# Performance work log

Hardware: AMD Instinct MI355X
Metric: run time of the kernel (lower is better)

The kernel has to match this reference:

```python
import jax, jax.numpy as jnp
import numpy as np

# ---- constants (from init_kwargs / Config) ----
C = 10            # number of classes
P = 128           # fixed prototype capacity per class (masked)
GAMMA = 0.1
B_CONST = 10.0    # b
TAO = 1.0
BETA = 1.0
LAMBDA = 0.1
THRESHOLD = 40.0
EPS = 1e-6        # nn.PairwiseDistance eps (added to the difference)


def setup_inputs() -> dict:
    key = jax.random.key(0)
    k1, k2 = jax.random.split(key)
    features = jax.random.normal(k1, (8192, 512), dtype=jnp.float32)
    labels = jax.random.randint(k2, (8192,), 0, C, dtype=jnp.int32)
    return {"features": features, "labels": labels}


def _assign_prototypes(features, labels):
    """Sequential prototype assignment (faithful to assign_prototype).
    Fixed-capacity store: protos [C,P,D], counts [C,P], nproto [C]."""
    D = features.shape[1]
    protos = jnp.zeros((C, P, D), features.dtype)
    counts = jnp.zeros((C, P), jnp.int32)
    nproto = jnp.zeros((C,), jnp.int32)

    def step(carry, xs):
        protos, counts, nproto = carry
        f, l = xs
        row = protos[l]                       # [P, D]
        cnt = counts[l]                       # [P]
        n = nproto[l]
        valid = jnp.arange(P) < n
        d2 = jnp.sum((f[None, :] - row + EPS) ** 2, axis=-1)
        d2m = jnp.where(valid, d2, jnp.inf)
        idx = jnp.argmin(d2m)
        dmin = jnp.sqrt(d2m[idx])
        do_update = (n > 0) & (dmin < THRESHOLD)
        # running-mean update of closest prototype
        c = cnt[idx].astype(f.dtype)
        new_val = (row[idx] * c + f) / (c + 1.0)
        app_idx = jnp.minimum(n, P - 1)       # append slot (clamped; never hit with these settings)
        tgt_idx = jnp.where(do_update, idx, app_idx)
        tgt_val = jnp.where(do_update, new_val, f)
        tgt_cnt = jnp.where(do_update, cnt[idx] + 1, 1)
        row = row.at[tgt_idx].set(tgt_val)
        cnt = cnt.at[tgt_idx].set(tgt_cnt)
        n = jnp.where(do_update, n, jnp.minimum(n + 1, P))
        protos = protos.at[l].set(row)
        counts = counts.at[l].set(cnt)
        nproto = nproto.at[l].set(n)
        return (protos, counts, nproto), None

    (protos, counts, nproto), _ = jax.lax.scan(step, (protos, counts, nproto), (features, labels))
    return protos, nproto


def _forward(features, labels):
    # assign_prototype uses tensor(features).detach() -> stop_gradient
    protos, nproto = _assign_prototypes(jax.lax.stop_gradient(features), labels)
    B, D = features.shape
    flat = protos.reshape(C * P, D)
    valid = (jnp.arange(P)[None, :] < nproto[:, None]).reshape(C * P)

    # squared PairwiseDistance with eps added to the difference:
    # sum((f - p + eps)^2) = |f|^2 + |p|^2 - 2 f.p + 2*eps*(sum f - sum p) + D*eps^2
    f2 = jnp.sum(features ** 2, axis=-1)          # [B]
    p2 = jnp.sum(flat ** 2, axis=-1)              # [C*P]
    sf = jnp.sum(features, axis=-1)
    sp = jnp.sum(flat, axis=-1)
    d2 = (f2[:, None] + p2[None, :] - 2.0 * (features @ flat.T)
          + 2.0 * EPS * (sf[:, None] - sp[None, :]) + D * EPS * EPS)
    d2 = jnp.maximum(d2, 0.0)                     # [B, C*P]

    # dce loss: probability = 1e-6 + sum_label exp(-g d^2) / sum_all exp(-g d^2)
    expv = jnp.where(valid[None, :], jnp.exp(-GAMMA * d2), 0.0)
    per_class = expv.reshape(B, C, P).sum(-1)     # [B, C]
    one = per_class.sum(-1)                       # [B]
    num = jnp.take_along_axis(per_class, labels[:, None].astype(jnp.int32), axis=1)[:, 0]
    prob = 1e-6 + jnp.where(one > 0.0, num / one, one)
    dce_loss = jnp.sum(-jnp.log(prob))

    # pairwise loss: per sample, per existing class, min distance
    d2c = jnp.where(valid[None, :], d2, jnp.inf).reshape(B, C, P).min(-1)
    dmin = jnp.sqrt(d2c)                          # [B, C]
    sign = jnp.where(labels[:, None] == jnp.arange(C)[None, :], 1.0, -1.0)
    z = B_CONST - (TAO - dmin) * sign
    g = jnp.where(z > 10.0, z, jax.nn.softplus(BETA * z) / BETA)
    exists = nproto > 0                           # only classes present in all_prototypes
    pw_loss = jnp.sum(jnp.where(exists[None, :], g, 0.0))

    return dce_loss + LAMBDA * pw_loss


def reference(features, labels):
    return _forward(features, labels)
```

## Files before the change

### kernel.cpp

```cpp
#include <hip/hip_runtime.h>
#include <math.h>

#define NC 10
#define NP 128
#define ND 512
#define GAMMA  0.1f
#define BCONST 10.0f
#define TAO    1.0f
#define LAMBDA 0.1f
#define THR2   1600.0f
#define FEPS   1e-6f
#define NLDS   12
#define CH     16
#define WPB    2
#define NBLK   261

__device__ __forceinline__ float allredf(float v) {
#pragma unroll
  for (int m = 1; m < 64; m <<= 1) v += __shfl_xor(v, m, 64);
  return v;
}

__global__ __launch_bounds__(256)
void sumc_kernel(const float* __restrict__ feats, const int* __restrict__ labels, int B,
                 float* __restrict__ chunksum, int* __restrict__ order_g,
                 int* __restrict__ cb_g, int* __restrict__ cc_g, int* __restrict__ chb_g,
                 int* __restrict__ ncht_g, int* __restrict__ done_g,
                 int* __restrict__ fail_g, int* __restrict__ nproto_g,
                 float* __restrict__ out)
{
  __shared__ unsigned int lab32[2048];
  __shared__ int list[8192];
  __shared__ int wtot[4][NC];
  __shared__ int cb_s[NC], cc_s[NC], chb_s[NC];
  __shared__ int nchtot_s;

  const int t = threadIdx.x, lane = t & 63, w = t >> 6;

  const int4* lp = (const int4*)labels;
  for (int i = t; i < (B >> 2); i += 256) {
    int4 v = lp[i];
    lab32[i] = (unsigned)(v.x & 255) | ((unsigned)(v.y & 255) << 8)
             | ((unsigned)(v.z & 255) << 16) | ((unsigned)(v.w & 255) << 24);
  }
  __syncthreads();

  const int segsz = (B + 255) >> 8;
  const int i0 = t * segsz, i1 = min(i0 + segsz, B);

  int loc[NC];
#pragma unroll
  for (int c = 0; c < NC; ++c) loc[c] = 0;
  for (int i = i0; i < i1; ++i) {
    int l = (int)((lab32[i >> 2] >> ((i & 3) * 8)) & 255u);
#pragma unroll
    for (int c = 0; c < NC; ++c) loc[c] += (l == c);
  }
  int pre[NC];
#pragma unroll
  for (int c = 0; c < NC; ++c) pre[c] = loc[c];
#pragma unroll
  for (int m = 1; m < 64; m <<= 1) {
#pragma unroll
    for (int c = 0; c < NC; ++c) {
      int u = __shfl_up(pre[c], m, 64);
      if (lane >= m) pre[c] += u;
    }
  }
  if (lane == 63) {
#pragma unroll
    for (int c = 0; c < NC; ++c) wtot[w][c] = pre[c];
  }
  __syncthreads();

  int pos[NC];
  {
    int cb = 0, crun = 0;
#pragma unroll
    for (int c = 0; c < NC; ++c) {
      int tot = wtot[0][c] + wtot[1][c] + wtot[2][c] + wtot[3][c];
      int before = 0;
#pragma unroll
      for (int ww = 0; ww < 4; ++ww) before += (ww < w) ? wtot[ww][c] : 0;
      pos[c] = cb + before + (pre[c] - loc[c]);
      if (t == 0) { cb_s[c] = cb; cc_s[c] = tot; chb_s[c] = crun; }
      cb += tot;
      crun += (tot + CH - 1) / CH;
    }
    if (t == 0) nchtot_s = crun;
  }
  for (int i = i0; i < i1; ++i) {
    int l = (int)((lab32[i >> 2] >> ((i & 3) * 8)) & 255u);
#pragma unroll
    for (int c = 0; c < NC; ++c)
      if (l == c) list[pos[c]++] = i;
  }
  __syncthreads();

  if (blockIdx.x < 4) {
    int q = (B + 3) >> 2;
    int lo = blockIdx.x * q, hi = min(lo + q, B);
    for (int i = lo + t; i < hi; i += 256) order_g[i] = list[i];
  }
  if (blockIdx.x == 0) {
    if (t < NC) {
      cb_g[t] = cb_s[t]; cc_g[t] = cc_s[t]; chb_g[t] = chb_s[t];
      done_g[t] = 0; fail_g[t] = 0; nproto_g[t] = 0;
    }
    if (t == 0) { ncht_g[0] = nchtot_s; out[0] = 0.f; }
  }

  if (w >= WPB) return;
  const int gwid = blockIdx.x * WPB + w;
  if (gwid >= nchtot_s) return;

  int c = 0;
  while (c + 1 < NC && chb_s[c + 1] <= gwid) ++c;
  const int g = gwid - chb_s[c];
  const int cnt = cc_s[c], base = cb_s[c];
  const int k0 = g * CH, k1 = min(k0 + CH, cnt);

  float S[8] = {0, 0, 0, 0, 0, 0, 0, 0};
  int k = k0;
  for (; k + 8 <= k1; k += 8) {
    float4 A[8], Bv[8];
#pragma unroll
    for (int j = 0; j < 8; ++j) {
      int idx = list[base + k + j];
      const float4* fp = (const float4*)(feats + (size_t)idx * ND + lane * 8);
      A[j] = fp[0]; Bv[j] = fp[1];
    }
#pragma unroll
    for (int j = 0; j < 8; ++j) {
      S[0]+=A[j].x; S[1]+=A[j].y; S[2]+=A[j].z; S[3]+=A[j].w;
      S[4]+=Bv[j].x; S[5]+=Bv[j].y; S[6]+=Bv[j].z; S[7]+=Bv[j].w;
    }
  }
  for (; k < k1; ++k) {
    int idx = list[base + k];
    const float4* fp = (const float4*)(feats + (size_t)idx * ND + lane * 8);
    float4 a = fp[0], b = fp[1];
    S[0]+=a.x; S[1]+=a.y; S[2]+=a.z; S[3]+=a.w;
    S[4]+=b.x; S[5]+=b.y; S[6]+=b.z; S[7]+=b.w;
  }
  float4* cp = (float4*)(chunksum + (size_t)gwid * ND + lane * 8);
  cp[0] = make_float4(S[0], S[1], S[2], S[3]);
  cp[1] = make_float4(S[4], S[5], S[6], S[7]);
}

__global__ __launch_bounds__(256)
void verify_kernel(const float* __restrict__ feats, int B,
                   const float* __restrict__ chunksum, const int* __restrict__ order_g,
                   const int* __restrict__ cb_g, const int* __restrict__ cc_g,
                   const int* __restrict__ chb_g, const int* __restrict__ ncht_g,
                   int* __restrict__ done_g, int* __restrict__ fail_g,
                   float* __restrict__ gproto, float* __restrict__ p2s,
                   float* __restrict__ sps, int* __restrict__ nproto_g)
{
  __shared__ int   cb_s[NC], cc_s[NC], chb_s[NC];
  __shared__ int   nchtot_s;
  __shared__ float ls_proto[NLDS][ND];
  __shared__ int   ls_cnt[NP];
  __shared__ int   fblock;

  const int t = threadIdx.x, lane = t & 63, w = t >> 6;
  if (t < NC) { cb_s[t] = cb_g[t]; cc_s[t] = cc_g[t]; chb_s[t] = chb_g[t]; }
  if (t == 32) nchtot_s = ncht_g[0];
  if (t == 33) fblock = 0;
  __syncthreads();

  if (w >= WPB) return;
  const int gwid = blockIdx.x * WPB + w;
  if (gwid >= nchtot_s) return;

  int c = 0;
  while (c + 1 < NC && chb_s[c + 1] <= gwid) ++c;
  const int g = gwid - chb_s[c];
  const int cnt = cc_s[c], base = cb_s[c];
  const int nchc = (cnt + CH - 1) / CH;
  const int k0 = g * CH, k1 = min(k0 + CH, cnt);
  int myidx = (lane < CH && k0 + lane < cnt) ? order_g[base + k0 + lane] : 0;

  float P[8] = {0, 0, 0, 0, 0, 0, 0, 0};
  {
    const float* cbase = chunksum + (size_t)chb_s[c] * ND + lane * 8;
    int j = 0;
    for (; j + 8 <= g; j += 8) {
      float4 A[8], Bv[8];
#pragma unroll
      for (int q = 0; q < 8; ++q) {
        const float4* pp = (const float4*)(cbase + (size_t)(j + q) * ND);
        A[q] = pp[0]; Bv[q] = pp[1];
      }
#pragma unroll
      for (int q = 0; q < 8; ++q) {
        P[0]+=A[q].x; P[1]+=A[q].y; P[2]+=A[q].z; P[3]+=A[q].w;
        P[4]+=Bv[q].x; P[5]+=Bv[q].y; P[6]+=Bv[q].z; P[7]+=Bv[q].w;
      }
    }
    for (; j < g; ++j) {
      const float4* pp = (const float4*)(cbase + (size_t)j * ND);
      float4 a = pp[0], b = pp[1];
      P[0]+=a.x; P[1]+=a.y; P[2]+=a.z; P[3]+=a.w;
      P[4]+=b.x; P[5]+=b.y; P[6]+=b.z; P[7]+=b.w;
    }
  }

  int k = k0;
  for (; k + 8 <= k1; k += 8) {
    float4 A[8], Bv[8];
#pragma unroll
    for (int j = 0; j < 8; ++j) {
      int idx = __shfl(myidx, k + j - k0, 64);
      const float4* fp = (const float4*)(feats + (size_t)idx * ND + lane * 8);
      A[j] = fp[0]; Bv[j] = fp[1];
    }
    float part[8];
#pragma unroll
    for (int j = 0; j < 8; ++j) {
      int kk = k + j;
      float f[8] = {A[j].x, A[j].y, A[j].z, A[j].w, Bv[j].x, Bv[j].y, Bv[j].z, Bv[j].w};
      if (kk > 0) {
        float invk = 1.f / (float)kk;
        float p = 0.f;
#pragma unroll
        for (int e = 0; e < 8; ++e) { float d = f[e] - P[e] * invk + FEPS; p += d * d; }
        part[j] = p;
      } else part[j] = 0.f;
#pragma unroll
      for (int e = 0; e < 8; ++e) P[e] += f[e];
    }
#pragma unroll
    for (int m = 1; m < 64; m <<= 1) {
#pragma unroll
      for (int j = 0; j < 8; ++j) part[j] += __shfl_xor(part[j], m, 64);
    }
    if (lane == 0) {
#pragma unroll
      for (int j = 0; j < 8; ++j) {
        int kk = k + j;
        if (kk > 0 && !(part[j] < THR2)) atomicOr(&fail_g[c], 1);
      }
    }
  }
  for (; k < k1; ++k) {
    int idx = __shfl(myidx, k - k0, 64);
    const float4* fp = (const float4*)(feats + (size_t)idx * ND + lane * 8);
    float4 fa = fp[0], fb = fp[1];
    float f[8] = {fa.x, fa.y, fa.z, fa.w, fb.x, fb.y, fb.z, fb.w};
    if (k > 0) {
      float invk = 1.f / (float)k;
      float p = 0.f;
#pragma unroll
      for (int e = 0; e < 8; ++e) { float d = f[e] - P[e] * invk + FEPS; p += d * d; }
      float d2 = allredf(p);
      if (!(d2 < THR2) && lane == 0) atomicOr(&fail_g[c], 1);
    }
#pragma unroll
    for (int e = 0; e < 8; ++e) P[e] += f[e];
  }

  if (g == nchc - 1) {
    float invc = 1.f / (float)cnt;
    float p[8];
#pragma unroll
    for (int e = 0; e < 8; ++e) p[e] = P[e] * invc;
    float4* gp = (float4*)(gproto + (size_t)c * NP * ND + lane * 8);
    gp[0] = make_float4(p[0], p[1], p[2], p[3]);
    gp[1] = make_float4(p[4], p[5], p[6], p[7]);
    float P2p = 0.f, SPp = 0.f;
#pragma unroll
    for (int e = 0; e < 8; ++e) { P2p += p[e]*p[e]; SPp += p[e]; }
    float P2 = allredf(P2p), SP = allredf(SPp);
    if (lane == 0) { p2s[c*NP] = P2; sps[c*NP] = SP; nproto_g[c] = 1; }
  }

  __threadfence();
  int old = 0;
  if (lane == 0) old = atomicAdd(&done_g[c], 1);
  old = __shfl(old, 0, 64);
  if (old != nchc - 1) return;
  __threadfence();
  int fv = 0;
  if (lane == 0) fv = atomicOr(&fail_g[c], 0);
  fv = __shfl(fv, 0, 64);
  if (!fv) return;

  if (lane == 0) { while (atomicCAS(&fblock, 0, 1) != 0) {} }

  {
    float p0[8];
    int cnt0 = 0, n = 0;
    float fA[8], fB[8], fC[8];

    auto LOADF = [&](float (&buf)[8], int m) {
      int idx = order_g[base + m];
      const float4* fp = (const float4*)(feats + (size_t)idx * ND + lane * 8);
      float4 a = fp[0], b = fp[1];
      buf[0]=a.x; buf[1]=a.y; buf[2]=a.z; buf[3]=a.w;
      buf[4]=b.x; buf[5]=b.y; buf[6]=b.z; buf[7]=b.w;
    };
    auto STEP = [&](float (&f)[8]) {
      float best = 3.4e38f;
      int bidx = 0;
      if (n > 0) {
        float part = 0.f;
#pragma unroll
        for (int e = 0; e < 8; ++e) { float d = f[e] - p0[e] + FEPS; part += d * d; }
        best = allredf(part);
        for (int j = 1; j < n; ++j) {
          float pj[8];
          if (j <= NLDS) {
            const float4* pp = (const float4*)(&ls_proto[j-1][lane*8]);
            float4 a = pp[0], b = pp[1];
            pj[0]=a.x; pj[1]=a.y; pj[2]=a.z; pj[3]=a.w;
            pj[4]=b.x; pj[5]=b.y; pj[6]=b.z; pj[7]=b.w;
          } else {
            const float4* pp = (const float4*)(gproto + ((size_t)c*NP + j)*ND + lane*8);
            float4 a = pp[0], b = pp[1];
            pj[0]=a.x; pj[1]=a.y; pj[2]=a.z; pj[3]=a.w;
            pj[4]=b.x; pj[5]=b.y; pj[6]=b.z; pj[7]=b.w;
          }
          float part2 = 0.f;
#pragma unroll
          for (int e = 0; e < 8; ++e) { float d = f[e] - pj[e] + FEPS; part2 += d * d; }
          float tot = allredf(part2);
          if (tot < best) { best = tot; bidx = j; }
        }
      }
      if (n > 0 && best < THR2) {
        if (bidx == 0) {
          float cc = (float)cnt0, iv = 1.f / (cc + 1.f);
#pragma unroll
          for (int e = 0; e < 8; ++e) p0[e] = (p0[e]*cc + f[e]) * iv;
          cnt0++;
        } else {
          int ci = ls_cnt[bidx];
          float cc = (float)ci, iv = 1.f / (cc + 1.f);
          if (bidx <= NLDS) {
            float* row = &ls_proto[bidx-1][lane*8];
#pragma unroll
            for (int e = 0; e < 8; ++e) row[e] = (row[e]*cc + f[e]) * iv;
          } else {
            float* row = gproto + ((size_t)c*NP + bidx)*ND + lane*8;
#pragma unroll
            for (int e = 0; e < 8; ++e) row[e] = (row[e]*cc + f[e]) * iv;
          }
          if (lane == 0) ls_cnt[bidx] = ci + 1;
        }
      } else {
        int app = min(n, NP - 1);
        if (app == 0) {
#pragma unroll
          for (int e = 0; e < 8; ++e) p0[e] = f[e];
          cnt0 = 1;
        } else if (app <= NLDS) {
          float* row = &ls_proto[app-1][lane*8];
#pragma unroll
          for (int e = 0; e < 8; ++e) row[e] = f[e];
          if (lane == 0) ls_cnt[app] = 1;
        } else {
          float* row = gproto + ((size_t)c*NP + app)*ND + lane*8;
#pragma unroll
          for (int e = 0; e < 8; ++e) row[e] = f[e];
          if (lane == 0) ls_cnt[app] = 1;
        }
        n = min(n + 1, NP);
      }
    };

    if (cnt > 0) LOADF(fA, 0);
    if (cnt > 1) LOADF(fB, 1);
    if (cnt > 2) LOADF(fC, 2);
    int m = 0;
    while (m < cnt) {
      STEP(fA); ++m; if (m + 2 < cnt) LOADF(fA, m + 2);
      if (m >= cnt) break;
      STEP(fB); ++m; if (m + 2 < cnt) LOADF(fB, m + 2);
      if (m >= cnt) break;
      STEP(fC); ++m; if (m + 2 < cnt) LOADF(fC, m + 2);
    }

    for (int j = 0; j < n; ++j) {
      float pj[8];
      if (j == 0) {
#pragma unroll
        for (int e = 0; e < 8; ++e) pj[e] = p0[e];
      } else if (j <= NLDS) {
        const float4* pp = (const float4*)(&ls_proto[j-1][lane*8]);
        float4 a = pp[0], b = pp[1];
        pj[0]=a.x; pj[1]=a.y; pj[2]=a.z; pj[3]=a.w;
        pj[4]=b.x; pj[5]=b.y; pj[6]=b.z; pj[7]=b.w;
      } else {
        const float4* pp = (const float4*)(gproto + ((size_t)c*NP + j)*ND + lane*8);
        float4 a = pp[0], b = pp[1];
        pj[0]=a.x; pj[1]=a.y; pj[2]=a.z; pj[3]=a.w;
        pj[4]=b.x; pj[5]=b.y; pj[6]=b.z; pj[7]=b.w;
      }
      float4* gp = (float4*)(gproto + ((size_t)c*NP + j)*ND + lane*8);
      gp[0] = make_float4(pj[0], pj[1], pj[2], pj[3]);
      gp[1] = make_float4(pj[4], pj[5], pj[6], pj[7]);
      float P2p = 0.f, SPp = 0.f;
#pragma unroll
      for (int e = 0; e < 8; ++e) { P2p += pj[e]*pj[e]; SPp += pj[e]; }
      float P2 = allredf(P2p), SP = allredf(SPp);
      if (lane == 0) { p2s[c*NP + j] = P2; sps[c*NP + j] = SP; }
    }
    if (lane == 0) nproto_g[c] = n;
  }

  __threadfence_block();
  if (lane == 0) atomicExch(&fblock, 0);
}

__global__ __launch_bounds__(256)
void loss_kernel(const float* __restrict__ feats, const int* __restrict__ labels, int B,
                 const float* __restrict__ gproto, const float* __restrict__ p2s,
                 const float* __restrict__ sps, const int* __restrict__ nproto_g,
                 float* __restrict__ out)
{
  __shared__ float bsum[4];
  const int lane = threadIdx.x & 63;
  const int wid  = threadIdx.x >> 6;
  const int gw   = blockIdx.x * 4 + wid;
  const int nw   = gridDim.x * 4;

  int np[NC];
  bool fast = true;
#pragma unroll
  for (int cc = 0; cc < NC; ++cc) { np[cc] = nproto_g[cc]; fast &= (np[cc] == 1); }

  float acc = 0.f;
  if (fast) {
    float p2v[NC], spv[NC];
#pragma unroll
    for (int cc = 0; cc < NC; ++cc) { p2v[cc] = p2s[cc*NP]; spv[cc] = sps[cc*NP]; }
    for (int b = gw; b < B; b += nw) {
      const float4* fp = (const float4*)(feats + (size_t)b * ND + lane * 8);
      float4 a4 = fp[0], b4 = fp[1];
      float f[8] = {a4.x, a4.y, a4.z, a4.w, b4.x, b4.y, b4.z, b4.w};
      int lab = labels[b];
      float v[12];
#pragma unroll
      for (int cc = 0; cc < NC; ++cc) {
        const float4* pp = (const float4*)(gproto + (size_t)cc * NP * ND + lane * 8);
        float4 pa = pp[0], pb = pp[1];
        v[cc] = f[0]*pa.x + f[1]*pa.y + f[2]*pa.z + f[3]*pa.w
              + f[4]*pb.x + f[5]*pb.y + f[6]*pb.z + f[7]*pb.w;
      }
      float f2p = 0.f, sfp = 0.f;
#pragma unroll
      for (int e = 0; e < 8; ++e) { f2p += f[e]*f[e]; sfp += f[e]; }
      v[10] = f2p; v[11] = sfp;
#pragma unroll
      for (int m = 1; m < 64; m <<= 1) {
#pragma unroll
        for (int q = 0; q < 12; ++q) v[q] += __shfl_xor(v[q], m, 64);
      }
      float f2 = v[10], sf = v[11];
      float one = 0.f, num = 0.f, pw = 0.f;
#pragma unroll
      for (int cc = 0; cc < NC; ++cc) {
        float d2 = f2 + p2v[cc] - 2.f*v[cc]
                 + 2.f*FEPS*(sf - spv[cc]) + (float)ND*FEPS*FEPS;
        d2 = fmaxf(d2, 0.f);
        float e = expf(-GAMMA * d2);
        one += e;
        if (cc == lab) num = e;
        float dmin = sqrtf(d2);
        float sign = (cc == lab) ? 1.f : -1.f;
        float z = BCONST - (TAO - dmin) * sign;
        float gg = (z > 10.f) ? z : log1pf(expf(z));
        pw += gg;
      }
      float prob = 1e-6f + ((one > 0.f) ? num / one : one);
      acc += -logf(prob) + LAMBDA * pw;
    }
  } else {
    for (int b = gw; b < B; b += nw) {
      const float4* fp = (const float4*)(feats + (size_t)b * ND + lane * 8);
      float4 a4 = fp[0], b4 = fp[1];
      float f[8] = {a4.x, a4.y, a4.z, a4.w, b4.x, b4.y, b4.z, b4.w};
      float f2p = 0.f, sfp = 0.f;
#pragma unroll
      for (int e = 0; e < 8; ++e) { f2p += f[e]*f[e]; sfp += f[e]; }
      float f2 = allredf(f2p);
      float sf = allredf(sfp);
      int lab = labels[b];
      float one = 0.f, num = 0.f, pw = 0.f;
      for (int cc = 0; cc < NC; ++cc) {
        int nn = np[cc];
        if (nn <= 0) continue;
        float sume = 0.f, bestd2 = 3.4e38f;
        for (int j = 0; j < nn; ++j) {
          const float4* pp = (const float4*)(gproto + ((size_t)cc*NP + j)*ND + lane*8);
          float4 pa = pp[0], pb = pp[1];
          float dp = f[0]*pa.x + f[1]*pa.y + f[2]*pa.z + f[3]*pa.w
                   + f[4]*pb.x + f[5]*pb.y + f[6]*pb.z + f[7]*pb.w;
          float dot = allredf(dp);
          float d2 = f2 + p2s[cc*NP + j] - 2.f*dot
                   + 2.f*FEPS*(sf - sps[cc*NP + j]) + (float)ND*FEPS*FEPS;
          d2 = fmaxf(d2, 0.f);
          sume  += expf(-GAMMA * d2);
          bestd2 = fminf(bestd2, d2);
        }
        one += sume;
        if (cc == lab) num = sume;
        float dmin = sqrtf(bestd2);
        float sign = (cc == lab) ? 1.f : -1.f;
        float z = BCONST - (TAO - dmin) * sign;
        float g = (z > 10.f) ? z : log1pf(expf(z));
        pw += g;
      }
      float prob = 1e-6f + ((one > 0.f) ? num / one : one);
      acc += -logf(prob) + LAMBDA * pw;
    }
  }

  if (lane == 0) bsum[wid] = acc;
  __syncthreads();
  if (threadIdx.x == 0) atomicAdd(out, bsum[0] + bsum[1] + bsum[2] + bsum[3]);
}

extern "C" void kernel_launch(void* const* d_in, const int* in_sizes, int n_in,
                              void* d_out, int out_size, void* d_ws, size_t ws_size,
                              hipStream_t stream) {
  const float* feats  = (const float*)d_in[0];
  const int*   labels = (const int*)d_in[1];
  int B = in_sizes[0] / ND;
  const int maxwin = (B + CH - 1) / CH + NC;

  float* gproto   = (float*)d_ws;
  float* p2s      = gproto + (size_t)NC * NP * ND;
  float* sps      = p2s + NC * NP;
  float* chunksum = sps + NC * NP;
  int*   order_g  = (int*)(chunksum + (size_t)maxwin * ND);
  int*   cb_g     = order_g + B;
  int*   cc_g     = cb_g + NC;
  int*   chb_g    = cc_g + NC;
  int*   ncht_g   = chb_g + NC;
  int*   done_g   = ncht_g + 1;
  int*   fail_g   = done_g + NC;
  int*   nproto_g = fail_g + NC;
  float* outf     = (float*)d_out;

  hipLaunchKernelGGL(sumc_kernel, dim3(NBLK), dim3(256), 0, stream,
                     feats, labels, B, chunksum, order_g, cb_g, cc_g, chb_g,
                     ncht_g, done_g, fail_g, nproto_g, outf);
  hipLaunchKernelGGL(verify_kernel, dim3(NBLK), dim3(256), 0, stream,
                     feats, B, chunksum, order_g, cb_g, cc_g, chb_g, ncht_g,
                     done_g, fail_g, gproto, p2s, sps, nproto_g);
  hipLaunchKernelGGL(loss_kernel, dim3(2048), dim3(256), 0, stream,
                     feats, labels, B, gproto, p2s, sps, nproto_g, outf);
}
```

Before: 79.28 us.

## Stage prototypes in LDS and process four samples per wave in loss kernel

```diff
diff --git a/kernel.cpp b/kernel.cpp
--- a/kernel.cpp
+++ b/kernel.cpp
@@ -419,9 +419,12 @@
                  const float* __restrict__ sps, const int* __restrict__ nproto_g,
                  float* __restrict__ out)
 {
+  __shared__ float lsp[NC][ND];
+  __shared__ float lp2[NC], lsv[NC];
   __shared__ float bsum[4];
-  const int lane = threadIdx.x & 63;
-  const int wid  = threadIdx.x >> 6;
+  const int t = threadIdx.x;
+  const int lane = t & 63;
+  const int wid  = t >> 6;
   const int gw   = blockIdx.x * 4 + wid;
   const int nw   = gridDim.x * 4;
 
@@ -432,49 +435,76 @@
 
   float acc = 0.f;
   if (fast) {
-    float p2v[NC], spv[NC];
-#pragma unroll
-    for (int cc = 0; cc < NC; ++cc) { p2v[cc] = p2s[cc*NP]; spv[cc] = sps[cc*NP]; }
-    for (int b = gw; b < B; b += nw) {
-      const float4* fp = (const float4*)(feats + (size_t)b * ND + lane * 8);
-      float4 a4 = fp[0], b4 = fp[1];
-      float f[8] = {a4.x, a4.y, a4.z, a4.w, b4.x, b4.y, b4.z, b4.w};
-      int lab = labels[b];
-      float v[12];
+    for (int i = t; i < NC * (ND / 4); i += 256) {
+      int cc = i / (ND / 4), off = i % (ND / 4);
+      ((float4*)&lsp[cc][0])[off] = ((const float4*)(gproto + (size_t)cc * NP * ND))[off];
+    }
+    if (t < NC) { lp2[t] = p2s[t * NP]; lsv[t] = sps[t * NP]; }
+    __syncthreads();
+
+    for (int b0 = gw * 4; b0 < B; b0 += nw * 4) {
+      const int ns = min(4, B - b0);
+      float f[32];
+      int lab[4];
+#pragma unroll
+      for (int s = 0; s < 4; ++s) {
+        int b = b0 + ((s < ns) ? s : 0);
+        const float4* fp = (const float4*)(feats + (size_t)b * ND + lane * 8);
+        float4 a4 = fp[0], b4 = fp[1];
+        f[s*8+0]=a4.x; f[s*8+1]=a4.y; f[s*8+2]=a4.z; f[s*8+3]=a4.w;
+        f[s*8+4]=b4.x; f[s*8+5]=b4.y; f[s*8+6]=b4.z; f[s*8+7]=b4.w;
+        lab[s] = labels[b];
+      }
+
+      float v[48];
 #pragma unroll
       for (int cc = 0; cc < NC; ++cc) {
-        const float4* pp = (const float4*)(gproto + (size_t)cc * NP * ND + lane * 8);
+        const float4* pp = (const float4*)(&lsp[cc][lane * 8]);
         float4 pa = pp[0], pb = pp[1];
-        v[cc] = f[0]*pa.x + f[1]*pa.y + f[2]*pa.z + f[3]*pa.w
-              + f[4]*pb.x + f[5]*pb.y + f[6]*pb.z + f[7]*pb.w;
-      }
-      float f2p = 0.f, sfp = 0.f;
-#pragma unroll
-      for (int e = 0; e < 8; ++e) { f2p += f[e]*f[e]; sfp += f[e]; }
-      v[10] = f2p; v[11] = sfp;
+        float p[8] = {pa.x, pa.y, pa.z, pa.w, pb.x, pb.y, pb.z, pb.w};
+#pragma unroll
+        for (int s = 0; s < 4; ++s) {
+          float d = 0.f;
+#pragma unroll
+          for (int e = 0; e < 8; ++e) d += f[s*8+e] * p[e];
+          v[s*12+cc] = d;
+        }
+      }
+#pragma unroll
+      for (int s = 0; s < 4; ++s) {
+        float f2p = 0.f, sfp = 0.f;
+#pragma unroll
+        for (int e = 0; e < 8; ++e) { f2p += f[s*8+e]*f[s*8+e]; sfp += f[s*8+e]; }
+        v[s*12+10] = f2p; v[s*12+11] = sfp;
+      }
 #pragma unroll
       for (int m = 1; m < 64; m <<= 1) {
 #pragma unroll
-        for (int q = 0; q < 12; ++q) v[q] += __shfl_xor(v[q], m, 64);
-      }
-      float f2 = v[10], sf = v[11];
-      float one = 0.f, num = 0.f, pw = 0.f;
-#pragma unroll
-      for (int cc = 0; cc < NC; ++cc) {
-        float d2 = f2 + p2v[cc] - 2.f*v[cc]
-                 + 2.f*FEPS*(sf - spv[cc]) + (float)ND*FEPS*FEPS;
-        d2 = fmaxf(d2, 0.f);
-        float e = expf(-GAMMA * d2);
-        one += e;
-        if (cc == lab) num = e;
-        float dmin = sqrtf(d2);
-        float sign = (cc == lab) ? 1.f : -1.f;
-        float z = BCONST - (TAO - dmin) * sign;
-        float gg = (z > 10.f) ? z : log1pf(expf(z));
-        pw += gg;
-      }
-      float prob = 1e-6f + ((one > 0.f) ? num / one : one);
-      acc += -logf(prob) + LAMBDA * pw;
+        for (int q = 0; q < 48; ++q) v[q] += __shfl_xor(v[q], m, 64);
+      }
+
+#pragma unroll
+      for (int s = 0; s < 4; ++s) {
+        if (s >= ns) break;
+        float f2 = v[s*12+10], sf = v[s*12+11];
+        float one = 0.f, num = 0.f, pw = 0.f;
+#pragma unroll
+        for (int cc = 0; cc < NC; ++cc) {
+          float d2 = f2 + lp2[cc] - 2.f*v[s*12+cc]
+                   + 2.f*FEPS*(sf - lsv[cc]) + (float)ND*FEPS*FEPS;
+          d2 = fmaxf(d2, 0.f);
+          float e = expf(-GAMMA * d2);
+          one += e;
+          if (cc == lab[s]) num = e;
+          float dmin = sqrtf(d2);
+          float sign = (cc == lab[s]) ? 1.f : -1.f;
+          float z = BCONST - (TAO - dmin) * sign;
+          float gg = (z > 10.f) ? z : log1pf(expf(z));
+          pw += gg;
+        }
+        float prob = 1e-6f + ((one > 0.f) ? num / one : one);
+        acc += -logf(prob) + LAMBDA * pw;
+      }
     }
   } else {
     for (int b = gw; b < B; b += nw) {
@@ -519,7 +549,7 @@
 
   if (lane == 0) bsum[wid] = acc;
   __syncthreads();
-  if (threadIdx.x == 0) atomicAdd(out, bsum[0] + bsum[1] + bsum[2] + bsum[3]);
+  if (t == 0) atomicAdd(out, bsum[0] + bsum[1] + bsum[2] + bsum[3]);
 }
 
 extern "C" void kernel_launch(void* const* d_in, const int* in_sizes, int n_in,
@@ -550,6 +580,6 @@
   hipLaunchKernelGGL(verify_kernel, dim3(NBLK), dim3(256), 0, stream,
                      feats, B, chunksum, order_g, cb_g, cc_g, chb_g, ncht_g,
                      done_g, fail_g, gproto, p2s, sps, nproto_g);
-  hipLaunchKernelGGL(loss_kernel, dim3(2048), dim3(256), 0, stream,
+  hipLaunchKernelGGL(loss_kernel, dim3(512), dim3(256), 0, stream,
                      feats, labels, B, gproto, p2s, sps, nproto_g, outf);
 }
```

New measurement: 78.26 us. No clear change (-1.3%).
